# Kernel optimization log

Hardware: AMD Instinct MI355X
Metric: run time of the kernel (lower is better)

Reference implementation:

```python
import jax, jax.numpy as jnp
import numpy as np

TEMPERATURE = 0.07
EPS = 1e-20

def setup_inputs() -> dict:
    key = jax.random.key(0)
    k1, k2 = jax.random.split(key)
    B, D, L = 4096, 256, 20
    features = jax.random.normal(k1, (B, D), dtype=jnp.float32)
    labels = jax.random.randint(k2, (B, L), 0, 5)
    return {"features": features, "labels": labels}

def reference(features, labels):
    B = features.shape[0]
    dt = features.dtype
    # [B, B] similarity logits, numerically stabilized (max is detached in torch)
    logits = (features @ features.T) / TEMPERATURE
    logits = logits - jax.lax.stop_gradient(jnp.max(logits, axis=1, keepdims=True))
    logits_mask = 1.0 - jnp.eye(B, dtype=dt)  # exclude self-contrast
    # shared across all label columns (the torch loop recomputes this each iter)
    exp_sum = jnp.sum(jnp.exp(logits) * logits_mask, axis=1, keepdims=True)
    log_prob = logits - jnp.log(exp_sum + EPS)

    def per_label(carry, lab):  # lab: [B] labels for one time-step
        mask = (lab[:, None] == lab[None, :]).astype(dt) * logits_mask  # [B, B]
        pos = mask.sum(1)                                   # positives per anchor
        single = (pos == 0).astype(dt)                      # anchors with no positives
        mean_lp = (mask * log_prob).sum(1) / (pos + single)
        loss_vec = -mean_lp * (1.0 - single)
        loss_i = loss_vec.sum() / (jnp.asarray(B, dt) - single.sum())
        return carry, loss_i

    _, losses = jax.lax.scan(per_label, jnp.float32(0.0), labels.T)  # [L]
    # torch fills minute_loss[:, i] with the scalar loss_i, then takes mean -> mean over i
    return jnp.mean(losses)
```

## Files before the change

### kernel.cpp

```cpp
#include <hip/hip_runtime.h>


#define B_N 4096
#define D_K 256
#define L_N 20
#define INVT 14.285714285714286f

#define CNT_OFF  0x004000u
#define WT_OFF   0x010000u
#define ACC_OFF  0x029000u
#define MPT_OFF  0x030000u
#define EPT_OFF  0x130000u

typedef __bf16 bf16x8 __attribute__((ext_vector_type(8)));
typedef float f32x4 __attribute__((ext_vector_type(4)));

struct __align__(16) U4 { unsigned int x, y, z, w; };

__device__ __forceinline__ unsigned int f2bf(float x) {
  unsigned int u = __float_as_uint(x);
  return (u + 0x7FFFu + ((u >> 16) & 1u)) >> 16;
}

__device__ __forceinline__ U4 pack8(float4 a, float4 b) {
  U4 r;
  r.x = f2bf(a.x) | (f2bf(a.y) << 16);
  r.y = f2bf(a.z) | (f2bf(a.w) << 16);
  r.z = f2bf(b.x) | (f2bf(b.y) << 16);
  r.w = f2bf(b.z) | (f2bf(b.w) << 16);
  return r;
}

__global__ __launch_bounds__(512, 2) void k_fused(const float* __restrict__ F,
                                                  const int* __restrict__ lab,
                                                  unsigned char* __restrict__ ws) {
  __shared__ unsigned char smem[75776];
  const int bid = blockIdx.x, t = threadIdx.x;
  if (bid < 256) {
    const int w = t >> 6, l = t & 63;
    const int lr = l & 15, lg = l >> 4;
    const int r = bid & 7, s = bid >> 3;
    const int bm = ((r & 3) << 1) | (s & 1);
    const int bn = ((r >> 2) << 4) | (s >> 1);
    const int rowbase = bm * 512 + w * 64;
    const int colb = bn * 128;
    {
      const int srow = t >> 2, q = t & 3;
      const float* src = F + (colb + srow) * 256 + q * 64;
      #pragma unroll
      for (int i = 0; i < 8; ++i) {
        float4 f0 = *(const float4*)(src + i * 8);
        float4 f1 = *(const float4*)(src + i * 8 + 4);
        const int kb = q * 128 + i * 16;
        *(U4*)(smem + srow * 512 + (kb ^ ((srow & 7) << 4))) = pack8(f0, f1);
      }
    }
    __syncthreads();
    float* MPT = (float*)(ws + MPT_OFF);
    float* EPT = (float*)(ws + EPT_OFF);
    float* scv = (float*)(smem + 73728);
    const float* arow0 = F + (rowbase + lr) * 256 + lg * 8;
    float ssq[4] = {0.f, 0.f, 0.f, 0.f};
    #pragma unroll 1
    for (int tile = 0; tile < 2; ++tile) {
      f32x4 acc[4][4] = {};
      #pragma unroll 1
      for (int kk = 0; kk < 8; ++kk) {
        bf16x8 afr[4];
        #pragma unroll
        for (int mi = 0; mi < 4; ++mi) {
          const float* ap = arow0 + mi * 16 * 256 + kk * 32;
          float4 a0 = *(const float4*)(ap);
          float4 a1 = *(const float4*)(ap + 4);
          if (tile == 0)
            ssq[mi] += a0.x * a0.x + a0.y * a0.y + a0.z * a0.z + a0.w * a0.w
                     + a1.x * a1.x + a1.y * a1.y + a1.z * a1.z + a1.w * a1.w;
          afr[mi] = __builtin_bit_cast(bf16x8, pack8(a0, a1));
        }
        bf16x8 bfr[4];
        #pragma unroll
        for (int n = 0; n < 4; ++n) {
          const int brow = tile * 64 + n * 16 + lr;
          const int kb = kk * 64 + lg * 16;
          bfr[n] = __builtin_bit_cast(bf16x8,
              *(const U4*)(smem + brow * 512 + (kb ^ ((brow & 7) << 4))));
        }
        #pragma unroll
        for (int mi = 0; mi < 4; ++mi)
          #pragma unroll
          for (int n = 0; n < 4; ++n)
            acc[mi][n] = __builtin_amdgcn_mfma_f32_16x16x32_bf16(afr[mi], bfr[n], acc[mi][n], 0, 0, 0);
      }
      if (tile == 0) {
        #pragma unroll
        for (int mi = 0; mi < 4; ++mi) {
          float ss = ssq[mi];
          ss += __shfl_xor(ss, 16, 64);
          ss += __shfl_xor(ss, 32, 64);
          if (lg == 0) scv[w * 64 + mi * 16 + lr] = ss * INVT;
        }
      }
      float2* scr = (float2*)(smem + 65536 + (w * 2 + tile) * 512);
      #pragma unroll
      for (int mi = 0; mi < 4; ++mi) {
        #pragma unroll
        for (int rr = 0; rr < 4; ++rr) {
          const int row = rowbase + mi * 16 + lg * 4 + rr;
          const float crow = scv[w * 64 + mi * 16 + lg * 4 + rr];
          float vm = -3.4e38f, es = 0.f;
          #pragma unroll
          for (int n = 0; n < 4; ++n) {
            const int col = colb + tile * 64 + n * 16 + lr;
            const float v = acc[mi][n][rr] * INVT;
            vm = fmaxf(vm, v);
            const float e = __expf(v - crow);
            es += (col == row) ? 0.f : e;
          }
          #pragma unroll
          for (int off = 1; off < 16; off <<= 1) {
            vm = fmaxf(vm, __shfl_xor(vm, off, 16));
            es += __shfl_xor(es, off, 16);
          }
          if (lr == 0) scr[mi * 16 + lg * 4 + rr] = make_float2(vm, es);
        }
      }
      const float2 v2 = scr[l];
      const int c2 = (colb >> 6) + tile;
      MPT[c2 * 4096 + rowbase + l] = v2.x;
      EPT[c2 * 4096 + rowbase + l] = v2.y;
    }
  } else if (bid < 276) {
    __shared__ int sc[8][5];
    const int l = bid - 256;
    int c0 = 0, c1 = 0, c2 = 0, c3 = 0, c4 = 0;
    for (int j = t; j < B_N; j += 512) {
      int v = lab[j * L_N + l];
      c0 += (v == 0); c1 += (v == 1); c2 += (v == 2); c3 += (v == 3); c4 += (v == 4);
    }
    #pragma unroll
    for (int off = 1; off < 64; off <<= 1) {
      c0 += __shfl_xor(c0, off, 64); c1 += __shfl_xor(c1, off, 64);
      c2 += __shfl_xor(c2, off, 64); c3 += __shfl_xor(c3, off, 64);
      c4 += __shfl_xor(c4, off, 64);
    }
    const int w = t >> 6;
    if ((t & 63) == 0) { sc[w][0] = c0; sc[w][1] = c1; sc[w][2] = c2; sc[w][3] = c3; sc[w][4] = c4; }
    __syncthreads();
    if (t < 5) {
      int s5 = 0;
      #pragma unroll
      for (int ww = 0; ww < 8; ++ww) s5 += sc[ww][t];
      ((int*)(ws + CNT_OFF))[l * 5 + t] = s5;
    }
  } else {
    int* slab = (int*)smem;
    const int idx = bid - 276;
    const int l = idx >> 3, jblk = idx & 7;
    const int j0 = jblk * 512;
    slab[t] = lab[(j0 + t) * L_N + l];
    __syncthreads();
    const int d = t & 255, half = t >> 8;
    const int base = half * 256;
    float a0 = 0, a1 = 0, a2 = 0, a3 = 0, a4 = 0;
    #pragma unroll 16
    for (int jj = 0; jj < 256; ++jj) {
      const int v = slab[base + jj];
      const float x = F[(j0 + base + jj) * 256 + d];
      a0 += (v == 0) ? x : 0.f;
      a1 += (v == 1) ? x : 0.f;
      a2 += (v == 2) ? x : 0.f;
      a3 += (v == 3) ? x : 0.f;
      a4 += (v == 4) ? x : 0.f;
    }
    float* Wt = (float*)(ws + WT_OFF);
    atomicAdd(Wt + (l * 5 + 0) * 256 + d, a0);
    atomicAdd(Wt + (l * 5 + 1) * 256 + d, a1);
    atomicAdd(Wt + (l * 5 + 2) * 256 + d, a2);
    atomicAdd(Wt + (l * 5 + 3) * 256 + d, a3);
    atomicAdd(Wt + (l * 5 + 4) * 256 + d, a4);
  }
}

__global__ __launch_bounds__(1024) void k_final(const float* __restrict__ F,
                                                const int* __restrict__ lab,
                                                unsigned char* __restrict__ ws,
                                                float* __restrict__ out) {
  __shared__ float WtL[25600];
  __shared__ float sL[16][20], sS[16][20];
  const int t = threadIdx.x, w = t >> 6, l = t & 63;
  const float* Wt = (const float*)(ws + WT_OFF);
  for (int s4 = t; s4 < 6400; s4 += 1024)
    *(float4*)(WtL + s4 * 4) = *(const float4*)(Wt + s4 * 4);
  __syncthreads();
  const int i = blockIdx.x * 16 + w;
  const float* MPT = (const float*)(ws + MPT_OFF);
  const float* EPT = (const float*)(ws + EPT_OFF);
  float m = MPT[l * 4096 + i];
  float e = EPT[l * 4096 + i];
  const float4 Ff = *(const float4*)(F + i * 256 + l * 4);
  float ci = Ff.x * Ff.x + Ff.y * Ff.y + Ff.z * Ff.z + Ff.w * Ff.w;
  #pragma unroll
  for (int off = 1; off < 64; off <<= 1) {
    m = fmaxf(m, __shfl_xor(m, off, 64));
    e += __shfl_xor(e, off, 64);
    ci += __shfl_xor(ci, off, 64);
  }
  ci *= INVT;
  const float lp = logf(e * __expf(ci - m) + 1e-20f);
  const int* cnts = (const int*)(ws + CNT_OFF);
  for (int ll = 0; ll < 20; ++ll) {
    const int v = lab[i * 20 + ll];
    const int cnt = cnts[ll * 5 + v] - 1;
    float lv = 0.f, sg = 0.f;
    if (cnt > 0) {
      const float4 Wf = *(const float4*)(WtL + (ll * 5 + v) * 256 + l * 4);
      float p = Ff.x * Wf.x + Ff.y * Wf.y + Ff.z * Wf.z + Ff.w * Wf.w;
      #pragma unroll
      for (int off = 1; off < 64; off <<= 1) p += __shfl_xor(p, off, 64);
      const float me = p * INVT - ci;
      lv = lp - (me - (float)cnt * m) / (float)cnt;
    } else {
      sg = 1.f;
    }
    if (l == 0) { sL[w][ll] = lv; sS[w][ll] = sg; }
  }
  __syncthreads();
  float* ACC = (float*)(ws + ACC_OFF);
  if (t < 20) {
    float Lsum = 0.f, Ssum = 0.f;
    #pragma unroll
    for (int ww = 0; ww < 16; ++ww) { Lsum += sL[ww][t]; Ssum += sS[ww][t]; }
    atomicAdd(ACC + t, Lsum);
    atomicAdd(ACC + 20 + t, Ssum);
  }
  __syncthreads();
  if (t == 0) {
    __threadfence();
    unsigned int done = atomicAdd((unsigned int*)(ws + ACC_OFF + 160), 1u);
    if (done == 255) {
      float v = 0.f;
      #pragma unroll
      for (int ll = 0; ll < 20; ++ll) {
        float Ls = __hip_atomic_load(ACC + ll, __ATOMIC_RELAXED, __HIP_MEMORY_SCOPE_AGENT);
        float Ss = __hip_atomic_load(ACC + 20 + ll, __ATOMIC_RELAXED, __HIP_MEMORY_SCOPE_AGENT);
        v += Ls / (4096.f - Ss);
      }
      out[0] = v * 0.05f;
    }
  }
}

extern "C" void kernel_launch(void* const* d_in, const int* in_sizes, int n_in,
                              void* d_out, int out_size, void* d_ws, size_t ws_size,
                              hipStream_t stream) {
  const float* F = (const float*)d_in[0];
  const int* lab = (const int*)d_in[1];
  unsigned char* ws = (unsigned char*)d_ws;
  float* out = (float*)d_out;
  hipMemsetAsync(ws + WT_OFF, 0, 102400 + 256, stream);
  k_fused<<<436, 512, 0, stream>>>(F, lab, ws);
  k_final<<<256, 1024, 0, stream>>>(F, lab, ws, out);
}
```

Measured before the change: 138.2 us.

## Reduce row max/expsum with global atomics and drop LDS staging of weights

Replaces the per-column-tile partial max/expsum arrays (64 partials per row, later reduced in the final kernel) with direct global atomics: an order-preserving uint atomicMax for the max and atomicAdd for the exp-sum. The final kernel reads one value per row and no longer copies the 100KB class-sum table into shared memory, reading it from global/L2 instead. It also switches bf16 packing to native conversions. This adds atomic contention on 4096 row addresses. It also adds a nondeterministic float summation order. Note that summing exps taken relative to each row's own diagonal is still consistent.

```diff
diff --git a/kernel.cpp b/kernel.cpp
--- a/kernel.cpp
+++ b/kernel.cpp
@@ -9,32 +9,33 @@
 #define CNT_OFF  0x004000u
 #define WT_OFF   0x010000u
 #define ACC_OFF  0x029000u
-#define MPT_OFF  0x030000u
-#define EPT_OFF  0x130000u
+#define MP_OFF   0x02A000u
+#define EP_OFF   0x02E000u
 
 typedef __bf16 bf16x8 __attribute__((ext_vector_type(8)));
 typedef float f32x4 __attribute__((ext_vector_type(4)));
 
 struct __align__(16) U4 { unsigned int x, y, z, w; };
 
-__device__ __forceinline__ unsigned int f2bf(float x) {
+__device__ __forceinline__ U4 pack8(float4 a, float4 b) {
+  bf16x8 v;
+  v[0] = (__bf16)a.x; v[1] = (__bf16)a.y; v[2] = (__bf16)a.z; v[3] = (__bf16)a.w;
+  v[4] = (__bf16)b.x; v[5] = (__bf16)b.y; v[6] = (__bf16)b.z; v[7] = (__bf16)b.w;
+  return __builtin_bit_cast(U4, v);
+}
+
+__device__ __forceinline__ unsigned int ordf(float x) {
   unsigned int u = __float_as_uint(x);
-  return (u + 0x7FFFu + ((u >> 16) & 1u)) >> 16;
-}
-
-__device__ __forceinline__ U4 pack8(float4 a, float4 b) {
-  U4 r;
-  r.x = f2bf(a.x) | (f2bf(a.y) << 16);
-  r.y = f2bf(a.z) | (f2bf(a.w) << 16);
-  r.z = f2bf(b.x) | (f2bf(b.y) << 16);
-  r.w = f2bf(b.z) | (f2bf(b.w) << 16);
-  return r;
+  return (u & 0x80000000u) ? ~u : (u | 0x80000000u);
+}
+__device__ __forceinline__ float ordinv(unsigned int o) {
+  return __uint_as_float((o & 0x80000000u) ? (o & 0x7FFFFFFFu) : ~o);
 }
 
 __global__ __launch_bounds__(512, 2) void k_fused(const float* __restrict__ F,
                                                   const int* __restrict__ lab,
                                                   unsigned char* __restrict__ ws) {
-  __shared__ unsigned char smem[75776];
+  __shared__ unsigned char smem[67584];
   const int bid = blockIdx.x, t = threadIdx.x;
   if (bid < 256) {
     const int w = t >> 6, l = t & 63;
@@ -56,9 +57,9 @@
       }
     }
     __syncthreads();
-    float* MPT = (float*)(ws + MPT_OFF);
-    float* EPT = (float*)(ws + EPT_OFF);
-    float* scv = (float*)(smem + 73728);
+    unsigned int* MP = (unsigned int*)(ws + MP_OFF);
+    float* EP = (float*)(ws + EP_OFF);
+    float* scv = (float*)(smem + 65536);
     const float* arow0 = F + (rowbase + lr) * 256 + lg * 8;
     float ssq[4] = {0.f, 0.f, 0.f, 0.f};
     #pragma unroll 1
@@ -100,7 +101,6 @@
           if (lg == 0) scv[w * 64 + mi * 16 + lr] = ss * INVT;
         }
       }
-      float2* scr = (float2*)(smem + 65536 + (w * 2 + tile) * 512);
       #pragma unroll
       for (int mi = 0; mi < 4; ++mi) {
         #pragma unroll
@@ -121,13 +121,12 @@
             vm = fmaxf(vm, __shfl_xor(vm, off, 16));
             es += __shfl_xor(es, off, 16);
           }
-          if (lr == 0) scr[mi * 16 + lg * 4 + rr] = make_float2(vm, es);
-        }
-      }
-      const float2 v2 = scr[l];
-      const int c2 = (colb >> 6) + tile;
-      MPT[c2 * 4096 + rowbase + l] = v2.x;
-      EPT[c2 * 4096 + rowbase + l] = v2.y;
+          if (lr == 0) {
+            atomicMax(MP + row, ordf(vm));
+            atomicAdd(EP + row, es);
+          }
+        }
+      }
     }
   } else if (bid < 276) {
     __shared__ int sc[8][5];
@@ -185,35 +184,25 @@
                                                 const int* __restrict__ lab,
                                                 unsigned char* __restrict__ ws,
                                                 float* __restrict__ out) {
-  __shared__ float WtL[25600];
   __shared__ float sL[16][20], sS[16][20];
   const int t = threadIdx.x, w = t >> 6, l = t & 63;
-  const float* Wt = (const float*)(ws + WT_OFF);
-  for (int s4 = t; s4 < 6400; s4 += 1024)
-    *(float4*)(WtL + s4 * 4) = *(const float4*)(Wt + s4 * 4);
-  __syncthreads();
   const int i = blockIdx.x * 16 + w;
-  const float* MPT = (const float*)(ws + MPT_OFF);
-  const float* EPT = (const float*)(ws + EPT_OFF);
-  float m = MPT[l * 4096 + i];
-  float e = EPT[l * 4096 + i];
   const float4 Ff = *(const float4*)(F + i * 256 + l * 4);
   float ci = Ff.x * Ff.x + Ff.y * Ff.y + Ff.z * Ff.z + Ff.w * Ff.w;
   #pragma unroll
-  for (int off = 1; off < 64; off <<= 1) {
-    m = fmaxf(m, __shfl_xor(m, off, 64));
-    e += __shfl_xor(e, off, 64);
-    ci += __shfl_xor(ci, off, 64);
-  }
+  for (int off = 1; off < 64; off <<= 1) ci += __shfl_xor(ci, off, 64);
   ci *= INVT;
+  const float m = ordinv(((const unsigned int*)(ws + MP_OFF))[i]);
+  const float e = ((const float*)(ws + EP_OFF))[i];
   const float lp = logf(e * __expf(ci - m) + 1e-20f);
+  const float* Wt = (const float*)(ws + WT_OFF);
   const int* cnts = (const int*)(ws + CNT_OFF);
   for (int ll = 0; ll < 20; ++ll) {
     const int v = lab[i * 20 + ll];
     const int cnt = cnts[ll * 5 + v] - 1;
     float lv = 0.f, sg = 0.f;
     if (cnt > 0) {
-      const float4 Wf = *(const float4*)(WtL + (ll * 5 + v) * 256 + l * 4);
+      const float4 Wf = *(const float4*)(Wt + (ll * 5 + v) * 256 + l * 4);
       float p = Ff.x * Wf.x + Ff.y * Wf.y + Ff.z * Wf.z + Ff.w * Wf.w;
       #pragma unroll
       for (int off = 1; off < 64; off <<= 1) p += __shfl_xor(p, off, 64);
@@ -257,7 +246,7 @@
   const int* lab = (const int*)d_in[1];
   unsigned char* ws = (unsigned char*)d_ws;
   float* out = (float*)d_out;
-  hipMemsetAsync(ws + WT_OFF, 0, 102400 + 256, stream);
+  hipMemsetAsync(ws + WT_OFF, 0, 0x22000, stream);
   k_fused<<<436, 512, 0, stream>>>(F, lab, ws);
   k_final<<<256, 1024, 0, stream>>>(F, lab, ws, out);
 }
```

Measured after the change: 138.7 us. No clear change (+0.4%).
